# Kernel tuning notes

Hardware: AMD Instinct MI355X
Metric: run time of the kernel (lower is better)

## Reference

```python
import jax, jax.numpy as jnp
import numpy as np
from jax import lax


def setup_inputs() -> dict:
    key = jax.random.key(0)
    k1, k2, k3, k4, k5 = jax.random.split(key, 5)
    B, T, D, N = 64, 1024, 512, 24
    return {
        "x": jax.random.normal(k1, (B, T, D), dtype=jnp.float32),
        "W": jax.random.normal(k2, (D, N), dtype=jnp.float32) * 0.05,
        "b": jnp.zeros((N,), dtype=jnp.float32),
        "trans": jax.random.normal(k3, (N, N), dtype=jnp.float32) * 0.1,
        "left_boundary": jax.random.normal(k4, (N,), dtype=jnp.float32) * 0.1,
        "right_boundary": jax.random.normal(k5, (N,), dtype=jnp.float32) * 0.1,
    }


def reference(x, W, b, trans, left_boundary, right_boundary):
    # Dense projection to tag potentials: [B, T, N]
    pot = jnp.einsum("btd,dn->btn", x, W) + b
    B, T, N = pot.shape
    # mask=None -> lengths are all T; boundaries added at t=0 and t=T-1
    lens = jnp.full((B,), T, dtype=jnp.int32)
    pot = pot.at[:, 0, :].add(left_boundary).at[:, T - 1, :].add(right_boundary)

    # Viterbi forward: alpha[b, j] = best score of any path ending in tag j
    def fwd_step(alpha, pot_t):
        scores = alpha[:, :, None] + trans[None, :, :]  # [B, prev, cur]
        bp = jnp.argmax(scores, axis=1)                 # [B, N] best prev tag
        alpha_new = jnp.max(scores, axis=1) + pot_t
        return alpha_new, bp

    alpha0 = pot[:, 0, :]
    pot_rest = jnp.swapaxes(pot[:, 1:, :], 0, 1)  # [T-1, B, N]
    alpha_T, bps = lax.scan(fwd_step, alpha0, pot_rest)
    last_tag = jnp.argmax(alpha_T, axis=-1)  # [B]

    # Backtrack through backpointers (reverse scan over time)
    def back_step(tag, bp_t):
        prev = jnp.take_along_axis(bp_t, tag[:, None], axis=1)[:, 0]
        return prev, prev

    _, tags_head = lax.scan(back_step, last_tag, bps, reverse=True)  # [T-1, B]
    decoded = jnp.concatenate(
        [jnp.swapaxes(tags_head, 0, 1), last_tag[:, None]], axis=1
    ).astype(jnp.int32)  # [B, T]
    return decoded, pot, lens, trans
```

## Files before the change

### kernel.cpp

```cpp
#include <hip/hip_runtime.h>
#include <hip/hip_bf16.h>

#define BB 64
#define TT 1024
#define DD 512
#define NS 24

#define POT_OFF   65536
#define LENS_OFF  1638400
#define TRANS_OFF 1638464

__global__ __launch_bounds__(256) void gemm_pot(
    const float* __restrict__ x, const float* __restrict__ W,
    const float* __restrict__ bias, const float* __restrict__ trans,
    const float* __restrict__ lb, const float* __restrict__ rb,
    float* __restrict__ out)
{
  __shared__ float wl[DD * NS];
  const int tid = threadIdx.x;
  const int l   = tid & 63;
  const int q   = tid >> 6;
  const int row0 = blockIdx.x * 128 + l;
  const int row1 = row0 + 64;

  {
    const float4* Ws = (const float4*)W;
    float4* Wd = (float4*)wl;
#pragma unroll
    for (int i = 0; i < 12; ++i) Wd[tid + i * 256] = Ws[tid + i * 256];
  }
  __syncthreads();

  const float4* xp0 = (const float4*)(x + (size_t)row0 * DD + q * 128);
  const float4* xp1 = (const float4*)(x + (size_t)row1 * DD + q * 128);

  float acc0[NS], acc1[NS];
#pragma unroll
  for (int nn = 0; nn < NS; ++nn) { acc0[nn] = 0.f; acc1[nn] = 0.f; }

  float4 buf0[4], buf1[4];
#pragma unroll
  for (int i = 0; i < 4; ++i) { buf0[i] = xp0[i]; buf1[i] = xp1[i]; }

#pragma unroll
  for (int f = 0; f < 32; ++f) {
    float4 v0 = buf0[f & 3];
    float4 v1 = buf1[f & 3];
    if (f + 4 < 32) { buf0[f & 3] = xp0[f + 4]; buf1[f & 3] = xp1[f + 4]; }
    const float xj0[4] = {v0.x, v0.y, v0.z, v0.w};
    const float xj1[4] = {v1.x, v1.y, v1.z, v1.w};
#pragma unroll
    for (int j = 0; j < 4; ++j) {
      const int k = q * 128 + f * 4 + j;
      const float4* wr = (const float4*)&wl[k * NS];
      float4 w0 = wr[0], w1 = wr[1], w2 = wr[2], w3 = wr[3], w4 = wr[4], w5 = wr[5];
      const float wv[NS] = {w0.x,w0.y,w0.z,w0.w, w1.x,w1.y,w1.z,w1.w,
                            w2.x,w2.y,w2.z,w2.w, w3.x,w3.y,w3.z,w3.w,
                            w4.x,w4.y,w4.z,w4.w, w5.x,w5.y,w5.z,w5.w};
      const float xv0 = xj0[j];
      const float xv1 = xj1[j];
#pragma unroll
      for (int nn = 0; nn < NS; ++nn) {
        acc0[nn] = fmaf(xv0, wv[nn], acc0[nn]);
        acc1[nn] = fmaf(xv1, wv[nn], acc1[nn]);
      }
    }
  }

  __syncthreads();
  if (q != 0) {
#pragma unroll
    for (int nn = 0; nn < NS; ++nn) {
      wl[((q - 1) * 128 + l)      * 25 + nn] = acc0[nn];
      wl[((q - 1) * 128 + 64 + l) * 25 + nn] = acc1[nn];
    }
  }
  __syncthreads();
  if (q == 0) {
#pragma unroll
    for (int rr = 0; rr < 2; ++rr) {
      float* acc = rr ? acc1 : acc0;
      const int row = rr ? row1 : row0;
      const int slot = rr ? (64 + l) : l;
      const int t = row & (TT - 1);
#pragma unroll
      for (int nn = 0; nn < NS; ++nn)
        acc[nn] += wl[(0 * 128 + slot) * 25 + nn] + wl[(1 * 128 + slot) * 25 + nn]
                 + wl[(2 * 128 + slot) * 25 + nn] + bias[nn];
      if (t == 0) {
#pragma unroll
        for (int nn = 0; nn < NS; ++nn) acc[nn] += lb[nn];
      }
      if (t == TT - 1) {
#pragma unroll
        for (int nn = 0; nn < NS; ++nn) acc[nn] += rb[nn];
      }
      float* po = out + POT_OFF + (size_t)row * NS;
#pragma unroll
      for (int i = 0; i < 6; ++i)
        *(float4*)(po + i * 4) = make_float4(acc[4*i], acc[4*i+1], acc[4*i+2], acc[4*i+3]);
    }
  }

  if (blockIdx.x == 0 && tid < BB) out[LENS_OFF + tid] = (float)TT;
  if (blockIdx.x == 1) {
    for (int i = tid; i < NS * NS; i += 256) out[TRANS_OFF + i] = trans[i];
  }
}

__device__ __forceinline__ float m3(float a, float b, float c) {
  return fmaxf(fmaxf(a, b), c);
}

#define RORI(dst, src, J) \
  dst = __builtin_amdgcn_mov_dpp((src), 0x120 + (J), 0xF, 0xF, true)

__global__ __launch_bounds__(1024) void viterbi_fused(
    const float* __restrict__ pot, const float* __restrict__ trans,
    float* __restrict__ out_dec)
{
  __shared__ float ps[TT * NS + 8];
  __shared__ unsigned char bl[TT * NS];
  __shared__ float tl[NS * NS];
  __shared__ int H[32][NS];
  __shared__ int e[32];

  const int b = blockIdx.x, tid = threadIdx.x;

  if (tid < NS * NS) tl[tid] = trans[tid];

  if (tid < 64) {
    const int r = tid >> 4;
    const int c = tid & 15;
    const int g = r >> 1;
    const int n = 16 * (r & 1) + c;
    const int nm = (n < NS) ? n : (NS - 1);

    const float* gp = pot + (size_t)b * TT * NS;

    int colv[16];
    colv[0] = c;
    RORI(colv[1],  c, 1);  RORI(colv[2],  c, 2);  RORI(colv[3],  c, 3);
    RORI(colv[4],  c, 4);  RORI(colv[5],  c, 5);  RORI(colv[6],  c, 6);
    RORI(colv[7],  c, 7);  RORI(colv[8],  c, 8);  RORI(colv[9],  c, 9);
    RORI(colv[10], c, 10); RORI(colv[11], c, 11); RORI(colv[12], c, 12);
    RORI(colv[13], c, 13); RORI(colv[14], c, 14); RORI(colv[15], c, 15);

    bool selx;
    {
      auto nr = __builtin_amdgcn_permlane16_swap(n, n, false, false);
      selx = (nr[0] == 16 * g + c);
    }

    float tcr[16];
#pragma unroll
    for (int j = 0; j < 16; ++j) {
      const int m = 16 * g + colv[j];
      tcr[j] = (m < NS) ? trans[m * NS + nm] : -__builtin_inff();
    }

    float ar[16];
#pragma unroll
    for (int j = 0; j < 16; ++j) {
      const int m = 16 * g + colv[j];
      ar[j] = gp[(m < NS) ? m : (NS - 1)];
    }

    ps[n] = gp[nm];

    float pv[8];
#pragma unroll
    for (int u = 0; u < 8; ++u) pv[u] = gp[(1 + u) * NS + nm];

    auto step = [&](int tt, float potv) {
      float sc[16];
#pragma unroll
      for (int j = 0; j < 16; ++j) sc[j] = ar[j] + tcr[j];
      float u0 = m3(sc[0],  sc[1],  sc[2]);
      float u1 = m3(sc[3],  sc[4],  sc[5]);
      float u2 = m3(sc[6],  sc[7],  sc[8]);
      float u3 = m3(sc[9],  sc[10], sc[11]);
      float u4 = m3(sc[12], sc[13], sc[14]);
      float pm = fmaxf(m3(u0, u1, u2), m3(u3, u4, sc[15]));
      auto pr = __builtin_amdgcn_permlane32_swap(
          __float_as_int(pm), __float_as_int(pm), false, false);
      float al = fmaxf(__int_as_float(pr[0]), __int_as_float(pr[1])) + potv;
      ps[tt * NS + n] = al;
      auto qr = __builtin_amdgcn_permlane16_swap(
          __float_as_int(al), __float_as_int(al), false, false);
      int asel = selx ? qr[0] : qr[1];
      ar[0] = __int_as_float(asel);
      int d1, d2, d3, d4, d5, d6, d7, d8, d9, d10, d11, d12, d13, d14, d15;
      RORI(d1,  asel, 1);  ar[1]  = __int_as_float(d1);
      RORI(d2,  asel, 2);  ar[2]  = __int_as_float(d2);
      RORI(d3,  asel, 3);  ar[3]  = __int_as_float(d3);
      RORI(d4,  asel, 4);  ar[4]  = __int_as_float(d4);
      RORI(d5,  asel, 5);  ar[5]  = __int_as_float(d5);
      RORI(d6,  asel, 6);  ar[6]  = __int_as_float(d6);
      RORI(d7,  asel, 7);  ar[7]  = __int_as_float(d7);
      RORI(d8,  asel, 8);  ar[8]  = __int_as_float(d8);
      RORI(d9,  asel, 9);  ar[9]  = __int_as_float(d9);
      RORI(d10, asel, 10); ar[10] = __int_as_float(d10);
      RORI(d11, asel, 11); ar[11] = __int_as_float(d11);
      RORI(d12, asel, 12); ar[12] = __int_as_float(d12);
      RORI(d13, asel, 13); ar[13] = __int_as_float(d13);
      RORI(d14, asel, 14); ar[14] = __int_as_float(d14);
      RORI(d15, asel, 15); ar[15] = __int_as_float(d15);
    };

    for (int t = 1; t + 7 <= TT - 1; t += 8) {
#pragma unroll
      for (int u = 0; u < 8; ++u) {
        const int tt = t + u;
        const float potv = pv[u];
        pv[u] = gp[(tt + 8) * NS + nm];
        step(tt, potv);
      }
    }
#pragma unroll
    for (int u = 0; u < 7; ++u) step(1017 + u, pv[u]);
  }
  __syncthreads();

  if (tid < 1008) {
    const int grp = tid / 24;
    const int n   = tid - grp * 24;
    float tlc[NS];
#pragma unroll
    for (int m = 0; m < NS; ++m) tlc[m] = tl[m * NS + n];
    for (int t = 1 + grp; t <= TT - 1; t += 42) {
      const float4* rr = (const float4*)&ps[(t - 1) * NS];
      float ar[NS];
#pragma unroll
      for (int i = 0; i < 6; ++i) {
        float4 v = rr[i];
        ar[4*i] = v.x; ar[4*i+1] = v.y; ar[4*i+2] = v.z; ar[4*i+3] = v.w;
      }
      float best = ar[0] + tlc[0];
      int bi = 0;
#pragma unroll
      for (int m = 1; m < NS; ++m) {
        float s = ar[m] + tlc[m];
        bool gg = s > best;
        bi = gg ? m : bi;
        best = gg ? s : best;
      }
      bl[t * NS + n] = (unsigned char)bi;
    }
  }
  __syncthreads();

  if (tid < 32 * NS) {
    const int c2 = tid / NS, s = tid % NS;
    int a2 = s;
    int tlo = c2 * 32; if (tlo < 1) tlo = 1;
    for (int t = c2 * 32 + 31; t >= tlo; --t) a2 = bl[t * NS + a2];
    H[c2][s] = a2;
  }
  __syncthreads();

  if (tid == 0) {
    const float* ar = &ps[(TT - 1) * NS];
    float best = ar[0]; int bi = 0;
#pragma unroll
    for (int nn = 1; nn < NS; ++nn) {
      float v = ar[nn];
      if (v > best) { best = v; bi = nn; }
    }
    int tag = bi;
    e[31] = tag;
    for (int c2 = 31; c2 >= 1; --c2) { tag = H[c2][tag]; e[c2 - 1] = tag; }
  }
  __syncthreads();

  if (tid < 32) {
    const int c2 = tid;
    int tag = e[c2];
    float* od = out_dec + (size_t)b * TT;
    od[c2 * 32 + 31] = (float)tag;
    for (int t = c2 * 32 + 30; t >= c2 * 32; --t) {
      tag = bl[(t + 1) * NS + tag];
      od[t] = (float)tag;
    }
  }
}

extern "C" void kernel_launch(void* const* d_in, const int* in_sizes, int n_in,
                              void* d_out, int out_size, void* d_ws, size_t ws_size,
                              hipStream_t stream)
{
  const float* x     = (const float*)d_in[0];
  const float* W     = (const float*)d_in[1];
  const float* bias  = (const float*)d_in[2];
  const float* trans = (const float*)d_in[3];
  const float* lb    = (const float*)d_in[4];
  const float* rb    = (const float*)d_in[5];
  float* out = (float*)d_out;

  gemm_pot<<<512, 256, 0, stream>>>(x, W, bias, trans, lb, rb, out);
  viterbi_fused<<<BB, 1024, 0, stream>>>(out + POT_OFF, trans, out);
}
```

Baseline: 321.6 us.

## Overlap backpointer computation with serial Viterbi forward via LDS progress flag

Instead of waiting for the whole forward recurrence to finish before computing argmax backpointers, the other 15 waves each own a time slice and spin on a shared progress counter published by the forward wave every 8 steps. They compute backpointers as soon as the alpha rows they need are ready. The forward wave's scheduling priority is also raised so it is not starved by the polling waves. This hides the backpointer phase behind the serial chain, at the cost of spin-wait overhead and reliance on ordering of LDS writes seen by other waves.

```diff
diff --git a/kernel.cpp b/kernel.cpp
--- a/kernel.cpp
+++ b/kernel.cpp
@@ -124,12 +124,16 @@
   __shared__ float tl[NS * NS];
   __shared__ int H[32][NS];
   __shared__ int e[32];
+  __shared__ int prog;
 
   const int b = blockIdx.x, tid = threadIdx.x;
 
   if (tid < NS * NS) tl[tid] = trans[tid];
+  if (tid == 0) *(volatile int*)&prog = 0;
+  __syncthreads();
 
   if (tid < 64) {
+    __builtin_amdgcn_s_setprio(1);
     const int r = tid >> 4;
     const int c = tid & 15;
     const int g = r >> 1;
@@ -216,36 +220,47 @@
         pv[u] = gp[(tt + 8) * NS + nm];
         step(tt, potv);
       }
+      asm volatile("" ::: "memory");
+      *(volatile int*)&prog = t + 7;
     }
 #pragma unroll
     for (int u = 0; u < 7; ++u) step(1017 + u, pv[u]);
-  }
-  __syncthreads();
-
-  if (tid < 1008) {
-    const int grp = tid / 24;
-    const int n   = tid - grp * 24;
+    asm volatile("" ::: "memory");
+    *(volatile int*)&prog = TT - 1;
+    __builtin_amdgcn_s_setprio(0);
+  } else {
+    const int w  = tid >> 6;
+    const int l  = tid & 63;
+    const int t0 = 1 + (w - 1) * 69;
+    const int tend = (t0 + 68 < TT - 1) ? (t0 + 68) : (TT - 1);
+    const int half = (l >= 24) ? 1 : 0;
+    const int n = (l < 24) ? l : ((l < 48) ? (l - 24) : 0);
     float tlc[NS];
 #pragma unroll
     for (int m = 0; m < NS; ++m) tlc[m] = tl[m * NS + n];
-    for (int t = 1 + grp; t <= TT - 1; t += 42) {
-      const float4* rr = (const float4*)&ps[(t - 1) * NS];
-      float ar[NS];
-#pragma unroll
-      for (int i = 0; i < 6; ++i) {
-        float4 v = rr[i];
-        ar[4*i] = v.x; ar[4*i+1] = v.y; ar[4*i+2] = v.z; ar[4*i+3] = v.w;
-      }
-      float best = ar[0] + tlc[0];
-      int bi = 0;
-#pragma unroll
-      for (int m = 1; m < NS; ++m) {
-        float s = ar[m] + tlc[m];
-        bool gg = s > best;
-        bi = gg ? m : bi;
-        best = gg ? s : best;
-      }
-      bl[t * NS + n] = (unsigned char)bi;
+    for (int ta = t0; ta <= tend; ta += 2) {
+      while (*(volatile int*)&prog < ta) __builtin_amdgcn_s_sleep(1);
+      asm volatile("" ::: "memory");
+      const int tloc = ta + half;
+      if (l < 48 && tloc <= tend) {
+        const float4* rr = (const float4*)&ps[(tloc - 1) * NS];
+        float arr[NS];
+#pragma unroll
+        for (int i = 0; i < 6; ++i) {
+          float4 v = rr[i];
+          arr[4*i] = v.x; arr[4*i+1] = v.y; arr[4*i+2] = v.z; arr[4*i+3] = v.w;
+        }
+        float best = arr[0] + tlc[0];
+        int bi = 0;
+#pragma unroll
+        for (int m = 1; m < NS; ++m) {
+          float s = arr[m] + tlc[m];
+          bool gg = s > best;
+          bi = gg ? m : bi;
+          best = gg ? s : best;
+        }
+        bl[tloc * NS + n] = (unsigned char)bi;
+      }
     }
   }
   __syncthreads();
```

Measured after the change: 317.4 us. About the same (-1.3%).
